# Optimization experiments

Hardware: AMD Instinct MI355X
Metric: run time of the kernel (lower is better)

Reference implementation:

```python
import jax, jax.numpy as jnp
import numpy as np

EPS_BN = 1e-5
EPS_LN = 1e-5

def _bn(x, gamma, beta, ch_axis):
    # training-mode BatchNorm: batch stats over all axes except ch_axis (biased var)
    axes = tuple(i for i in range(x.ndim) if i != ch_axis)
    mean = x.mean(axes, keepdims=True)
    var = x.var(axes, keepdims=True)
    shp = [1] * x.ndim; shp[ch_axis] = -1
    return (x - mean) / jnp.sqrt(var + EPS_BN) * gamma.reshape(shp) + beta.reshape(shp)

def _ln(x, gamma, beta):
    mean = x.mean(-1, keepdims=True)
    var = x.var(-1, keepdims=True)
    return (x - mean) / jnp.sqrt(var + EPS_LN) * gamma + beta

def _spline(x, knots, cps):
    # x: (B,S); knots, cps: (K,). Single-pass bucketize + gather + lerp,
    # equivalent to the torch per-interval masked loop (boundary points take
    # the right interval's t=0 value, identical result).
    K = knots.shape[0]
    xn = (x - jnp.min(x)) / (jnp.max(x) - jnp.min(x) + 1e-6)
    idx = jnp.clip(jnp.searchsorted(knots, xn, side='right') - 1, 0, K - 2)
    k0, k1 = knots[idx], knots[idx + 1]
    t = (xn - k0) / (k1 - k0)
    val = (1.0 - t) * cps[idx] + t * cps[idx + 1]
    in_range = (xn >= knots[0]) & (xn <= knots[-1])
    return jnp.where(in_range, val, 0.0)

def _mha(x, in_w, in_b, out_w, out_b, H):
    # torch nn.MultiheadAttention with batch_first=False: dim0 is the sequence.
    L, N, D = x.shape
    hd = D // H
    qkv = x @ in_w.T + in_b                       # (L,N,3D)
    q, k, v = jnp.split(qkv, 3, axis=-1)
    q = q.reshape(L, N, H, hd) * (1.0 / np.sqrt(hd))
    k = k.reshape(L, N, H, hd)
    v = v.reshape(L, N, H, hd)
    scores = jnp.einsum('lnhd,mnhd->nhlm', q, k)  # (N,H,L,L)
    attn = jax.nn.softmax(scores, axis=-1)
    out = jnp.einsum('nhlm,mnhd->lnhd', attn, v).reshape(L, N, D)
    return out @ out_w.T + out_b

def setup_inputs() -> dict:
    B, S, D, F, K, H = 32, 1024, 512, 8, 32, 8
    key = jax.random.key(0)
    ks = jax.random.split(key, 12)
    s = 0.02
    inp = {
        'x': jax.random.normal(ks[0], (B, S, D), jnp.float32),
        'in_w': jax.random.normal(ks[1], (3 * D, D), jnp.float32) * s,
        'in_b': jnp.zeros((3 * D,), jnp.float32),
        'out_w': jax.random.normal(ks[2], (D, D), jnp.float32) * s,
        'out_b': jnp.zeros((D,), jnp.float32),
        'attn_g': jnp.ones((D,), jnp.float32),
        'attn_beta': jnp.zeros((D,), jnp.float32),
        'proj_w': jax.random.normal(ks[3], (F, D), jnp.float32) * s,
        'proj_b': jnp.zeros((F,), jnp.float32),
        'pn_g': jnp.ones((F,), jnp.float32),
        'pn_beta': jnp.zeros((F,), jnp.float32),
        'knots': jnp.tile(jnp.linspace(0.0, 1.0, K, dtype=jnp.float32)[None, :], (F, 1)),
        'cps': jax.random.normal(ks[4], (F, K), jnp.float32) / np.sqrt(K),
        'gate_w': jax.random.normal(ks[5], (2 * D, F), jnp.float32) * s,
        'gate_b': jnp.zeros((2 * D,), jnp.float32),
        'gbn_g': jnp.ones((S,), jnp.float32),   # BatchNorm1d(2*d_model) hits dim1 = seq (= 2*d_model)
        'gbn_beta': jnp.zeros((S,), jnp.float32),
        'ln_g': jnp.ones((D,), jnp.float32),
        'ln_beta': jnp.zeros((D,), jnp.float32),
        'outp_w': jax.random.normal(ks[6], (D, D), jnp.float32) * s,
        'outp_b': jnp.zeros((D,), jnp.float32),
        'on_g': jnp.ones((D,), jnp.float32),
        'on_beta': jnp.zeros((D,), jnp.float32),
    }
    return inp

def reference(x, in_w, in_b, out_w, out_b, attn_g, attn_beta, proj_w, proj_b,
              pn_g, pn_beta, knots, cps, gate_w, gate_b, gbn_g, gbn_beta,
              ln_g, ln_beta, outp_w, outp_b, on_g, on_beta):
    H = 8
    attn_out = _mha(x, in_w, in_b, out_w, out_b, H)          # (B,S,D)
    attn_out = _bn(attn_out, attn_g, attn_beta, 2)
    projected = x @ proj_w.T + proj_b                         # (B,S,F)
    projected = _bn(projected, pn_g, pn_beta, 2)
    transformed = jax.vmap(_spline, in_axes=(2, 0, 0), out_axes=2)(projected, knots, cps)  # (B,S,F)
    h = transformed @ gate_w.T + gate_b                       # (B,S,2D)
    h = _bn(h, gbn_g, gbn_beta, 1)                            # channel axis = seq (torch quirk)
    a, b = jnp.split(h, 2, axis=-1)
    glu = a * jax.nn.sigmoid(b)                               # (B,S,D)
    gated = _ln(glu, ln_g, ln_beta)
    out = gated @ outp_w.T + outp_b
    out = _bn(out, on_g, on_beta, 2)
    return x + attn_out + out
```

## Files before the change

### kernel.cpp

```cpp
#include <hip/hip_runtime.h>
#include <math.h>


#define SOFF_AMEAN 0
#define SOFF_ARSTD 512
#define SOFF_OMEAN 1024
#define SOFF_ORSTD 1536
#define SOFF_PMEAN 2048
#define SOFF_PRSTD 2056
#define SOFF_FMIN  2064
#define SOFF_FMAX  2072
#define SOFF_SMEAN 2080
#define SOFF_SRSTD 3104
#define SOFF_G1    4128
#define SOFF_GB    4136
#define SOFF_SGB   4144
#define SOFF_QGB   4145
#define SOFF_G2    4160
#define SOFF_PART  4224

typedef short bf16x8_t __attribute__((ext_vector_type(8)));
typedef float f32x4_t __attribute__((ext_vector_type(4)));
typedef unsigned short us8_t __attribute__((ext_vector_type(8)));

__device__ __forceinline__ unsigned short f2bf(float f) {
  unsigned u = __float_as_uint(f);
  u = (u + 0x7FFFu + ((u >> 16) & 1u)) >> 16;
  return (unsigned short)u;
}
__device__ __forceinline__ float b2f(unsigned short u) {
  return __uint_as_float(((unsigned)u) << 16);
}

#define BARR do { asm volatile("" ::: "memory"); __builtin_amdgcn_s_barrier(); asm volatile("" ::: "memory"); } while (0)

__global__ __launch_bounds__(256) void zero_kernel(float* __restrict__ p) {
  p[blockIdx.x * 256 + threadIdx.x] = 0.f;
}

__global__ __launch_bounds__(256) void cvt8_kernel(const float* __restrict__ src,
                                                   unsigned short* __restrict__ dst) {
  int i = blockIdx.x * 256 + threadIdx.x;
  float4 a = ((const float4*)src)[i * 2];
  float4 b = ((const float4*)src)[i * 2 + 1];
  us8_t o;
  o[0] = f2bf(a.x); o[1] = f2bf(a.y); o[2] = f2bf(a.z); o[3] = f2bf(a.w);
  o[4] = f2bf(b.x); o[5] = f2bf(b.y); o[6] = f2bf(b.z); o[7] = f2bf(b.w);
  *(us8_t*)(dst + (size_t)i * 8) = o;
}

template<int NT, bool OUT_BF16, bool STATS>
__global__ __launch_bounds__(512, 2) void gemm256_kernel(
    const unsigned short* __restrict__ A, const unsigned short* __restrict__ B,
    const float* __restrict__ bias, unsigned short* __restrict__ Cb,
    float* __restrict__ Cf, float* __restrict__ gstats, int N) {
  __shared__ unsigned short As[4][256 * 32];
  __shared__ unsigned short Bs[4][256 * 32];
  const int bi = blockIdx.x;
  const int xcd = bi & 7, jb = bi >> 3;
  const int m0 = (xcd * 16 + jb / NT) * 256;
  const int n0 = (jb % NT) * 256;
  const int t = threadIdx.x;
  const int w = t >> 6, lane = t & 63;
  const int wm = w >> 2, wn = w & 3;

  const unsigned short* gA = A + (size_t)(m0 + w * 16 + (lane >> 2)) * 512
                               + (((lane & 3) ^ ((lane >> 3) & 3)) * 8);
  const unsigned short* gB = B + (size_t)(n0 + w * 16 + (lane >> 2)) * 512
                               + (((lane & 3) ^ ((lane >> 3) & 3)) * 8);

  const int fr = lane & 15, g = lane >> 4;
  const int kf = (fr >> 1) & 3;

  f32x4_t acc[8][4];
#pragma unroll
  for (int i = 0; i < 8; ++i)
#pragma unroll
    for (int jj = 0; jj < 4; ++jj) acc[i][jj] = (f32x4_t){0.f, 0.f, 0.f, 0.f};

#define STAGE(KT) do { \
    __builtin_amdgcn_global_load_lds( \
        (const __attribute__((address_space(1))) void*)(gA + (KT) * 32), \
        (__attribute__((address_space(3))) void*)&As[(KT) & 3][(w * 16) * 32], 16, 0, 0); \
    __builtin_amdgcn_global_load_lds( \
        (const __attribute__((address_space(1))) void*)(gA + (KT) * 32 + 128 * 512), \
        (__attribute__((address_space(3))) void*)&As[(KT) & 3][(128 + w * 16) * 32], 16, 0, 0); \
    __builtin_amdgcn_global_load_lds( \
        (const __attribute__((address_space(1))) void*)(gB + (KT) * 32), \
        (__attribute__((address_space(3))) void*)&Bs[(KT) & 3][(w * 16) * 32], 16, 0, 0); \
    __builtin_amdgcn_global_load_lds( \
        (const __attribute__((address_space(1))) void*)(gB + (KT) * 32 + 128 * 512), \
        (__attribute__((address_space(3))) void*)&Bs[(KT) & 3][(128 + w * 16) * 32], 16, 0, 0); \
  } while (0)

  STAGE(0); STAGE(1); STAGE(2);
  asm volatile("s_waitcnt vmcnt(8)" ::: "memory");
  BARR;

#pragma unroll
  for (int kt = 0; kt < 16; ++kt) {
    if (kt < 13) STAGE(kt + 3);
    const unsigned short* asb = &As[kt & 3][0];
    const unsigned short* bsb = &Bs[kt & 3][0];
    bf16x8_t af[8], bf[4];
#pragma unroll
    for (int ni = 0; ni < 4; ++ni)
      bf[ni] = *(const bf16x8_t*)&bsb[(wn * 64 + ni * 16 + fr) * 32 + ((g ^ kf) * 8)];
#pragma unroll
    for (int mi = 0; mi < 8; ++mi)
      af[mi] = *(const bf16x8_t*)&asb[(wm * 128 + mi * 16 + fr) * 32 + ((g ^ kf) * 8)];
    __builtin_amdgcn_s_setprio(1);
#pragma unroll
    for (int mi = 0; mi < 8; ++mi)
#pragma unroll
      for (int ni = 0; ni < 4; ++ni)
        acc[mi][ni] = __builtin_amdgcn_mfma_f32_16x16x32_bf16(af[mi], bf[ni], acc[mi][ni], 0, 0, 0);
    __builtin_amdgcn_s_setprio(0);
    if (kt < 15) {
      if (kt <= 12)      asm volatile("s_waitcnt vmcnt(8)" ::: "memory");
      else if (kt == 13) asm volatile("s_waitcnt vmcnt(4)" ::: "memory");
      else               asm volatile("s_waitcnt vmcnt(0)" ::: "memory");
      BARR;
    }
  }
#undef STAGE

  const int cr = (lane >> 4) * 4, cc = lane & 15;
  float bv[4], lsum[4], lsq[4];
#pragma unroll
  for (int ni = 0; ni < 4; ++ni) {
    bv[ni] = bias[n0 + wn * 64 + ni * 16 + cc];
    lsum[ni] = 0.f; lsq[ni] = 0.f;
  }
#pragma unroll
  for (int mi = 0; mi < 8; ++mi) {
#pragma unroll
    for (int jj = 0; jj < 4; ++jj) {
      const size_t row = (size_t)(m0 + wm * 128 + mi * 16 + cr + jj);
#pragma unroll
      for (int ni = 0; ni < 4; ++ni) {
        int col = n0 + wn * 64 + ni * 16 + cc;
        float v = acc[mi][ni][jj] + bv[ni];
        if (OUT_BF16) Cb[row * N + col] = f2bf(v);
        else          Cf[row * N + col] = v;
        if (STATS) { lsum[ni] += v; lsq[ni] += v * v; }
      }
    }
  }
  if (STATS) {
#pragma unroll
    for (int ni = 0; ni < 4; ++ni) {
      float s = lsum[ni], q = lsq[ni];
      s += __shfl_xor(s, 16); s += __shfl_xor(s, 32);
      q += __shfl_xor(q, 16); q += __shfl_xor(q, 32);
      if (lane < 16) {
        int col = n0 + wn * 64 + ni * 16 + lane;
        atomicAdd(&gstats[col], s);
        atomicAdd(&gstats[512 + col], q);
      }
    }
  }
}

__global__ __launch_bounds__(512) void statsfin_kernel(const float* __restrict__ part,
                                                       float* __restrict__ stats, int off) {
  int t = threadIdx.x;
  float mean = part[t] / 32768.f;
  float var = part[512 + t] / 32768.f - mean * mean;
  stats[off + t] = mean;
  stats[off + 512 + t] = rsqrtf(var + 1e-5f);
}

__global__ __launch_bounds__(256) void attn2_kernel(const unsigned short* __restrict__ qkv,
                                                    unsigned short* __restrict__ ctxb) {
  const int n = blockIdx.x, h = blockIdx.y, t = threadIdx.x;
  __shared__ float qs[32 * 68], ks[32 * 68], vs[32 * 68], ss[32 * 33];
  const int l = t >> 3, j0 = (t & 7) * 8;
  size_t rowb = ((size_t)(l * 1024 + n)) * 1536 + h * 64 + j0;
  us8_t qv = *(const us8_t*)(qkv + rowb);
  us8_t kv = *(const us8_t*)(qkv + rowb + 512);
  us8_t vv = *(const us8_t*)(qkv + rowb + 1024);
#pragma unroll
  for (int j = 0; j < 8; ++j) {
    qs[l * 68 + j0 + j] = b2f(qv[j]) * 0.125f;
    ks[l * 68 + j0 + j] = b2f(kv[j]);
    vs[l * 68 + j0 + j] = b2f(vv[j]);
  }
  __syncthreads();
  for (int o = t; o < 1024; o += 256) {
    int ll = o >> 5, m = o & 31;
    const float4* q4 = (const float4*)&qs[ll * 68];
    const float4* k4 = (const float4*)&ks[m * 68];
    float s = 0.f;
#pragma unroll
    for (int dd = 0; dd < 16; ++dd) {
      float4 a = q4[dd], b = k4[dd];
      s += a.x * b.x + a.y * b.y + a.z * b.z + a.w * b.w;
    }
    ss[ll * 33 + m] = s;
  }
  __syncthreads();
  if (t < 32) {
    float mx = -3e38f;
    for (int m = 0; m < 32; ++m) mx = fmaxf(mx, ss[t * 33 + m]);
    float sum = 0.f;
    for (int m = 0; m < 32; ++m) { float e = __expf(ss[t * 33 + m] - mx); ss[t * 33 + m] = e; sum += e; }
    float inv = 1.f / sum;
    for (int m = 0; m < 32; ++m) ss[t * 33 + m] *= inv;
  }
  __syncthreads();
  float o[8] = {0.f, 0.f, 0.f, 0.f, 0.f, 0.f, 0.f, 0.f};
#pragma unroll 8
  for (int m = 0; m < 32; ++m) {
    float pm = ss[l * 33 + m];
    const float* vr = &vs[m * 68 + j0];
#pragma unroll
    for (int j = 0; j < 8; ++j) o[j] += pm * vr[j];
  }
  us8_t ov;
#pragma unroll
  for (int j = 0; j < 8; ++j) ov[j] = f2bf(o[j]);
  *(us8_t*)(ctxb + ((size_t)(l * 1024 + n)) * 512 + h * 64 + j0) = ov;
}

__global__ __launch_bounds__(256) void proj_kernel(const float* __restrict__ x,
    const float* __restrict__ pw, const float* __restrict__ pb, float* __restrict__ p) {
  int blk = blockIdx.x, t = threadIdx.x;
  int r0 = blk * 64;
  __shared__ float xsp[64 * 33];
  __shared__ float pwc[8 * 33];
  int l = t >> 2, fg = t & 3;
  float acc0 = 0.f, acc1 = 0.f;
  for (int k0 = 0; k0 < 512; k0 += 32) {
    __syncthreads();
    for (int i = t; i < 2048; i += 256) { int ll = i >> 5, kk = i & 31; xsp[ll * 33 + kk] = x[(size_t)(r0 + ll) * 512 + k0 + kk]; }
    { int ff = t >> 5, kk = t & 31; pwc[ff * 33 + kk] = pw[ff * 512 + k0 + kk]; }
    __syncthreads();
#pragma unroll 8
    for (int kk = 0; kk < 32; ++kk) {
      float xv = xsp[l * 33 + kk];
      acc0 += xv * pwc[(fg * 2) * 33 + kk];
      acc1 += xv * pwc[(fg * 2 + 1) * 33 + kk];
    }
  }
  float2 o; o.x = acc0 + pb[fg * 2]; o.y = acc1 + pb[fg * 2 + 1];
  *(float2*)&p[(r0 + l) * 8 + fg * 2] = o;
}

__global__ __launch_bounds__(256) void projstats_kernel(const float* __restrict__ p,
                                                        float* __restrict__ part) {
  int t = threadIdx.x, blk = blockIdx.x;
  int f = t & 7;
  float s = 0.f, s2 = 0.f;
  for (int r = blk * 32 + (t >> 3); r < 32768; r += 2048) { float v = p[r * 8 + f]; s += v; s2 += v * v; }
  __shared__ float red[256], red2[256];
  red[t] = s; red2[t] = s2; __syncthreads();
  for (int off = 128; off >= 8; off >>= 1) { if (t < off) { red[t] += red[t + off]; red2[t] += red2[t + off]; } __syncthreads(); }
  if (t < 8) { part[blk * 16 + t] = red[t]; part[blk * 16 + 8 + t] = red2[t]; }
}
__global__ void projfin_kernel(const float* __restrict__ part, float* __restrict__ stats) {
  int t = threadIdx.x;
  if (t < 8) {
    float s = 0.f, s2 = 0.f;
    for (int b = 0; b < 64; ++b) { s += part[b * 16 + t]; s2 += part[b * 16 + 8 + t]; }
    float mean = s / 32768.f;
    float var = s2 / 32768.f - mean * mean;
    stats[SOFF_PMEAN + t] = mean;
    stats[SOFF_PRSTD + t] = rsqrtf(var + 1e-5f);
  }
}

__global__ __launch_bounds__(256) void bnminmax_kernel(float* __restrict__ p,
    const float* __restrict__ stats, const float* __restrict__ png,
    const float* __restrict__ pnb, float* __restrict__ part) {
  int t = threadIdx.x, blk = blockIdx.x;
  int i0 = blk * 256 + t;
  int f = i0 & 7;
  float k1 = stats[SOFF_PRSTD + f] * png[f];
  float k0 = pnb[f] - stats[SOFF_PMEAN + f] * k1;
  float mn = 3e38f, mx = -3e38f;
  for (int i = i0; i < 262144; i += 16384) {
    float v = p[i] * k1 + k0;
    p[i] = v;
    mn = fminf(mn, v); mx = fmaxf(mx, v);
  }
  __shared__ float rmn[256], rmx[256];
  rmn[t] = mn; rmx[t] = mx; __syncthreads();
  for (int off = 128; off >= 8; off >>= 1) {
    if (t < off) { rmn[t] = fminf(rmn[t], rmn[t + off]); rmx[t] = fmaxf(rmx[t], rmx[t + off]); }
    __syncthreads();
  }
  if (t < 8) { part[blk * 16 + t] = rmn[t]; part[blk * 16 + 8 + t] = rmx[t]; }
}
__global__ void minmaxfin_kernel(const float* __restrict__ part, float* __restrict__ stats) {
  int t = threadIdx.x;
  if (t < 8) {
    float mn = 3e38f, mx = -3e38f;
    for (int b = 0; b < 64; ++b) { mn = fminf(mn, part[b * 16 + t]); mx = fmaxf(mx, part[b * 16 + 8 + t]); }
    stats[SOFF_FMIN + t] = mn;
    stats[SOFF_FMAX + t] = mx;
  }
}

__global__ __launch_bounds__(256) void spline_kernel(float* __restrict__ p,
    const float* __restrict__ knots, const float* __restrict__ cps,
    const float* __restrict__ stats) {
  __shared__ float ksh[8 * 33], csh[8 * 33];
  int t = threadIdx.x;
  { int f = t >> 5, j = t & 31; ksh[f * 33 + j] = knots[t]; csh[f * 33 + j] = cps[t]; }
  __syncthreads();
  int i = blockIdx.x * 256 + t;
  int f = i & 7;
  float xv = p[i];
  float mn = stats[SOFF_FMIN + f], mx = stats[SOFF_FMAX + f];
  float xn = (xv - mn) / (mx - mn + 1e-6f);
  const float* kn = &ksh[f * 33];
  const float* cp = &csh[f * 33];
  int pcnt = 0;
#pragma unroll
  for (int j = 0; j < 32; ++j) pcnt += (kn[j] <= xn) ? 1 : 0;
  int idx = pcnt - 1;
  idx = idx < 0 ? 0 : (idx > 30 ? 30 : idx);
  float k0v = kn[idx], k1v = kn[idx + 1];
  float tt = (xn - k0v) / (k1v - k0v);
  float val = (1.f - tt) * cp[idx] + tt * cp[idx + 1];
  bool inr = (xn >= kn[0]) && (xn <= kn[31]);
  p[i] = inr ? val : 0.f;
}

__global__ __launch_bounds__(256) void gateprep_kernel(const float* __restrict__ gw,
    const float* __restrict__ gb, float* __restrict__ stats) {
  int b = blockIdx.x, t = threadIdx.x;
  __shared__ float red[256];
  float s = 0.f;
  if (b < 64) {
    int f1 = b >> 3, f2 = b & 7;
    for (int j = t; j < 1024; j += 256) s += gw[j * 8 + f1] * gw[j * 8 + f2];
  } else if (b < 72) {
    int f = b - 64;
    for (int j = t; j < 1024; j += 256) s += gw[j * 8 + f];
  } else if (b < 80) {
    int f = b - 72;
    for (int j = t; j < 1024; j += 256) s += gb[j] * gw[j * 8 + f];
  } else if (b == 80) {
    for (int j = t; j < 1024; j += 256) s += gb[j];
  } else {
    for (int j = t; j < 1024; j += 256) s += gb[j] * gb[j];
  }
  red[t] = s; __syncthreads();
  for (int off = 128; off > 0; off >>= 1) { if (t < off) red[t] += red[t + off]; __syncthreads(); }
  if (t == 0) {
    float v = red[0];
    if (b < 64) stats[SOFF_G2 + b] = v;
    else if (b < 72) stats[SOFF_G1 + (b - 64)] = v;
    else if (b < 80) stats[SOFF_GB + (b - 72)] = v;
    else if (b == 80) stats[SOFF_SGB] = v;
    else stats[SOFF_QGB] = v;
  }
}

__global__ __launch_bounds__(256) void sstats_kernel(const float* __restrict__ tbuf,
                                                     float* __restrict__ stats) {
  int s = blockIdx.x, t = threadIdx.x;
  __shared__ float tv[256];
  __shared__ float red[256];
  __shared__ float T1[8];
  __shared__ float Ms[64];
  int b = t >> 3, f = t & 7;
  tv[t] = tbuf[(b * 1024 + s) * 8 + f];
  __syncthreads();
  red[t] = tv[t]; __syncthreads();
  for (int off = 128; off >= 8; off >>= 1) { if (t < off) red[t] += red[t + off]; __syncthreads(); }
  if (t < 8) T1[t] = red[t];
  if (t < 64) {
    int f1 = t >> 3, f2 = t & 7; float sM = 0.f;
    for (int bb = 0; bb < 32; ++bb) sM += tv[bb * 8 + f1] * tv[bb * 8 + f2];
    Ms[t] = sM;
  }
  __syncthreads();
  if (t == 0) {
    float sh = 0.f, s2 = 0.f;
    for (int ff = 0; ff < 8; ++ff) {
      sh += stats[SOFF_G1 + ff] * T1[ff];
      s2 += 2.f * stats[SOFF_GB + ff] * T1[ff];
    }
    sh += 32.f * stats[SOFF_SGB];
    for (int i = 0; i < 64; ++i) s2 += Ms[i] * stats[SOFF_G2 + i];
    s2 += 32.f * stats[SOFF_QGB];
    float mean = sh / 32768.f;
    float var = s2 / 32768.f - mean * mean;
    stats[SOFF_SMEAN + s] = mean;
    stats[SOFF_SRSTD + s] = rsqrtf(var + 1e-5f);
  }
}

__global__ __launch_bounds__(256) void gluln_kernel(const float* __restrict__ tbuf,
    const float* __restrict__ gw, const float* __restrict__ gb,
    const float* __restrict__ stats, const float* __restrict__ gbng,
    const float* __restrict__ gbnb, const float* __restrict__ lng,
    const float* __restrict__ lnb, unsigned short* __restrict__ gatedb) {
  const int t = threadIdx.x, wave = t >> 6, lane = t & 63;
  for (int rr = 0; rr < 4; ++rr) {
    const int r = blockIdx.x * 16 + wave * 4 + rr;
    const int s = r & 1023;
    float4 tA = *(const float4*)&tbuf[r * 8];
    float4 tB = *(const float4*)&tbuf[r * 8 + 4];
    float smean = stats[SOFF_SMEAN + s], srstd = stats[SOFF_SRSTD + s];
    float k1 = srstd * gbng[s];
    float k0 = gbnb[s] - smean * k1;
    float g[8];
    float sum = 0.f, sq = 0.f;
#pragma unroll
    for (int i = 0; i < 8; ++i) {
      int c = i * 64 + lane;
      float4 wa0 = *(const float4*)&gw[c * 8];
      float4 wa1 = *(const float4*)&gw[c * 8 + 4];
      float4 wb0 = *(const float4*)&gw[(c + 512) * 8];
      float4 wb1 = *(const float4*)&gw[(c + 512) * 8 + 4];
      float ha = tA.x * wa0.x + tA.y * wa0.y + tA.z * wa0.z + tA.w * wa0.w
               + tB.x * wa1.x + tB.y * wa1.y + tB.z * wa1.z + tB.w * wa1.w + gb[c];
      float hb = tA.x * wb0.x + tA.y * wb0.y + tA.z * wb0.z + tA.w * wb0.w
               + tB.x * wb1.x + tB.y * wb1.y + tB.z * wb1.z + tB.w * wb1.w + gb[c + 512];
      ha = ha * k1 + k0;
      hb = hb * k1 + k0;
      float gv = ha / (1.f + __expf(-hb));
      g[i] = gv; sum += gv; sq += gv * gv;
    }
#pragma unroll
    for (int m = 32; m >= 1; m >>= 1) { sum += __shfl_xor(sum, m); sq += __shfl_xor(sq, m); }
    float mean = sum * (1.f / 512.f);
    float rstd = rsqrtf(sq * (1.f / 512.f) - mean * mean + 1e-5f);
#pragma unroll
    for (int i = 0; i < 8; ++i) {
      int c = i * 64 + lane;
      gatedb[(size_t)r * 512 + c] = f2bf((g[i] - mean) * rstd * lng[c] + lnb[c]);
    }
  }
}

__global__ __launch_bounds__(256) void final_kernel(const float* __restrict__ x,
    const float* __restrict__ attn, const float* __restrict__ outl,
    const float* __restrict__ stats, const float* __restrict__ ag,
    const float* __restrict__ ab, const float* __restrict__ og,
    const float* __restrict__ ob, float* __restrict__ y) {
  int idx = blockIdx.x * 256 + threadIdx.x;
  int c4 = (idx & 127) * 4;
  float4 xv = ((const float4*)x)[idx];
  float4 av = ((const float4*)attn)[idx];
  float4 ov = ((const float4*)outl)[idx];
  float4 am = *(const float4*)&stats[SOFF_AMEAN + c4];
  float4 ar = *(const float4*)&stats[SOFF_ARSTD + c4];
  float4 om = *(const float4*)&stats[SOFF_OMEAN + c4];
  float4 orr = *(const float4*)&stats[SOFF_ORSTD + c4];
  float4 g1 = *(const float4*)&ag[c4];
  float4 b1 = *(const float4*)&ab[c4];
  float4 g2 = *(const float4*)&og[c4];
  float4 b2 = *(const float4*)&ob[c4];
  float4 o;
  o.x = xv.x + (av.x - am.x) * ar.x * g1.x + b1.x + (ov.x - om.x) * orr.x * g2.x + b2.x;
  o.y = xv.y + (av.y - am.y) * ar.y * g1.y + b1.y + (ov.y - om.y) * orr.y * g2.y + b2.y;
  o.z = xv.z + (av.z - am.z) * ar.z * g1.z + b1.z + (ov.z - om.z) * orr.z * g2.z + b2.z;
  o.w = xv.w + (av.w - am.w) * ar.w * g1.w + b1.w + (ov.w - om.w) * orr.w * g2.w + b2.w;
  ((float4*)y)[idx] = o;
}

extern "C" void kernel_launch(void* const* d_in, const int* in_sizes, int n_in,
                              void* d_out, int out_size, void* d_ws, size_t ws_size,
                              hipStream_t stream) {
  (void)in_sizes; (void)n_in; (void)out_size; (void)ws_size;
  const float* x        = (const float*)d_in[0];
  const float* in_w     = (const float*)d_in[1];
  const float* in_b     = (const float*)d_in[2];
  const float* out_w    = (const float*)d_in[3];
  const float* out_b    = (const float*)d_in[4];
  const float* attn_g   = (const float*)d_in[5];
  const float* attn_bt  = (const float*)d_in[6];
  const float* proj_w   = (const float*)d_in[7];
  const float* proj_b   = (const float*)d_in[8];
  const float* pn_g     = (const float*)d_in[9];
  const float* pn_bt    = (const float*)d_in[10];
  const float* knots    = (const float*)d_in[11];
  const float* cps      = (const float*)d_in[12];
  const float* gate_w   = (const float*)d_in[13];
  const float* gate_b   = (const float*)d_in[14];
  const float* gbn_g    = (const float*)d_in[15];
  const float* gbn_bt   = (const float*)d_in[16];
  const float* ln_g     = (const float*)d_in[17];
  const float* ln_bt    = (const float*)d_in[18];
  const float* outp_w   = (const float*)d_in[19];
  const float* outp_b   = (const float*)d_in[20];
  const float* on_g     = (const float*)d_in[21];
  const float* on_bt    = (const float*)d_in[22];

  float* out = (float*)d_out;
  unsigned short* xb      = (unsigned short*)d_ws;
  unsigned short* qkv_b   = xb + 16777216;
  unsigned short* ctx_b   = qkv_b + 50331648;
  unsigned short* wqkv_b  = ctx_b + 16777216;
  unsigned short* wout_b  = wqkv_b + 786432;
  unsigned short* woutp_b = wout_b + 262144;
  float* proj  = (float*)(woutp_b + 262144);
  float* stats = proj + 262144;
  float* part  = stats + SOFF_PART;
  float* partA  = part;
  float* partO  = part + 1024;
  float* partP  = part + 2048;
  float* partMM = part + 3072;
  float* attnf = (float*)qkv_b;
  unsigned short* gated_b = xb;

  zero_kernel<<<dim3(8), dim3(256), 0, stream>>>(part);
  cvt8_kernel<<<dim3(8192), dim3(256), 0, stream>>>(x, xb);
  cvt8_kernel<<<dim3(384), dim3(256), 0, stream>>>(in_w, wqkv_b);
  cvt8_kernel<<<dim3(128), dim3(256), 0, stream>>>(out_w, wout_b);
  cvt8_kernel<<<dim3(128), dim3(256), 0, stream>>>(outp_w, woutp_b);
  gemm256_kernel<6, true, false><<<dim3(768), dim3(512), 0, stream>>>(
      xb, wqkv_b, in_b, qkv_b, nullptr, nullptr, 1536);
  attn2_kernel<<<dim3(1024, 8), dim3(256), 0, stream>>>(qkv_b, ctx_b);
  gemm256_kernel<2, false, true><<<dim3(256), dim3(512), 0, stream>>>(
      ctx_b, wout_b, out_b, nullptr, attnf, partA, 512);
  statsfin_kernel<<<dim3(1), dim3(512), 0, stream>>>(partA, stats, SOFF_AMEAN);
  proj_kernel<<<dim3(512), dim3(256), 0, stream>>>(x, proj_w, proj_b, proj);
  projstats_kernel<<<dim3(64), dim3(256), 0, stream>>>(proj, partP);
  projfin_kernel<<<dim3(1), dim3(64), 0, stream>>>(partP, stats);
  bnminmax_kernel<<<dim3(64), dim3(256), 0, stream>>>(proj, stats, pn_g, pn_bt, partMM);
  minmaxfin_kernel<<<dim3(1), dim3(64), 0, stream>>>(partMM, stats);
  spline_kernel<<<dim3(1024), dim3(256), 0, stream>>>(proj, knots, cps, stats);
  gateprep_kernel<<<dim3(88), dim3(256), 0, stream>>>(gate_w, gate_b, stats);
  sstats_kernel<<<dim3(1024), dim3(256), 0, stream>>>(proj, stats);
  gluln_kernel<<<dim3(2048), dim3(256), 0, stream>>>(proj, gate_w, gate_b, stats,
                                                     gbn_g, gbn_bt, ln_g, ln_bt, gated_b);
  gemm256_kernel<2, false, true><<<dim3(256), dim3(512), 0, stream>>>(
      gated_b, woutp_b, outp_b, nullptr, out, partO, 512);
  statsfin_kernel<<<dim3(1), dim3(512), 0, stream>>>(partO, stats, SOFF_OMEAN);
  final_kernel<<<dim3(16384), dim3(256), 0, stream>>>(x, attnf, out, stats,
                                                      attn_g, attn_bt, on_g, on_bt, out);
}
```

Before: 522.5 us.

## Rewrite attention kernel as single-wavefront MFMA bf16 QK^T and PV

Replaces the 256-thread FP32 LDS-based attention kernel with a 64-lane single-wavefront kernel. It computes the 32x32 scores and the probability-times-V product with bf16 16x16x32 MFMA instructions, keeps Q and K fragments in registers, and transposes only V through a small LDS buffer. Softmax runs in registers using cross-lane shuffles, and the probabilities are repacked into MFMA operand layout with xor shuffles. This removes most LDS traffic and scalar FMA work per (batch, head) block. In exchange the probabilities are rounded to bf16, the lane-permutation logic is intricate, and the output stores are scattered 2-byte writes.

```diff
diff --git a/kernel.cpp b/kernel.cpp
--- a/kernel.cpp
+++ b/kernel.cpp
@@ -171,56 +171,120 @@
   stats[off + 512 + t] = rsqrtf(var + 1e-5f);
 }
 
-__global__ __launch_bounds__(256) void attn2_kernel(const unsigned short* __restrict__ qkv,
-                                                    unsigned short* __restrict__ ctxb) {
-  const int n = blockIdx.x, h = blockIdx.y, t = threadIdx.x;
-  __shared__ float qs[32 * 68], ks[32 * 68], vs[32 * 68], ss[32 * 33];
-  const int l = t >> 3, j0 = (t & 7) * 8;
-  size_t rowb = ((size_t)(l * 1024 + n)) * 1536 + h * 64 + j0;
-  us8_t qv = *(const us8_t*)(qkv + rowb);
-  us8_t kv = *(const us8_t*)(qkv + rowb + 512);
-  us8_t vv = *(const us8_t*)(qkv + rowb + 1024);
-#pragma unroll
-  for (int j = 0; j < 8; ++j) {
-    qs[l * 68 + j0 + j] = b2f(qv[j]) * 0.125f;
-    ks[l * 68 + j0 + j] = b2f(kv[j]);
-    vs[l * 68 + j0 + j] = b2f(vv[j]);
-  }
+__global__ __launch_bounds__(64) void attn3_kernel(const unsigned short* __restrict__ qkv,
+                                                   unsigned short* __restrict__ ctxb) {
+  const int n = blockIdx.x, h = blockIdx.y;
+  const int lane = threadIdx.x;
+  const int fr = lane & 15, g = lane >> 4;
+  const int r = lane & 31, hi2 = lane >> 5;
+  __shared__ unsigned short vt[64 * 32];
+
+  const unsigned short* base = qkv + (size_t)n * 1536 + (size_t)h * 64;
+
+#pragma unroll
+  for (int i = 0; i < 4; ++i) {
+    const int d0 = (i * 2 + hi2) * 8;
+    union { us8_t v; unsigned u[4]; } ov;
+    ov.v = *(const us8_t*)(base + (size_t)r * 1572864 + 1024 + d0);
+#pragma unroll
+    for (int w = 0; w < 4; ++w) {
+      unsigned o = ov.u[w];
+      unsigned pu = __shfl_xor(o, 1);
+      unsigned val = (r & 1) ? ((pu >> 16) | (o & 0xFFFF0000u))
+                             : ((o & 0xFFFFu) | (pu << 16));
+      int dw = d0 + 2 * w + (r & 1);
+      *(unsigned*)&vt[dw * 32 + (r >> 1) * 2] = val;
+    }
+  }
+
+  bf16x8_t kfr[2][2], qfr[2][2];
+#pragma unroll
+  for (int mi = 0; mi < 2; ++mi)
+#pragma unroll
+    for (int s = 0; s < 2; ++s)
+      kfr[mi][s] = *(const bf16x8_t*)(base + (size_t)(mi * 16 + fr) * 1572864 + 512 + s * 32 + g * 8);
+#pragma unroll
+  for (int li = 0; li < 2; ++li)
+#pragma unroll
+    for (int s = 0; s < 2; ++s)
+      qfr[li][s] = *(const bf16x8_t*)(base + (size_t)(li * 16 + fr) * 1572864 + s * 32 + g * 8);
+
+  f32x4_t st[2][2];
+#pragma unroll
+  for (int mi = 0; mi < 2; ++mi)
+#pragma unroll
+    for (int li = 0; li < 2; ++li) {
+      st[mi][li] = (f32x4_t){0.f, 0.f, 0.f, 0.f};
+#pragma unroll
+      for (int s = 0; s < 2; ++s)
+        st[mi][li] = __builtin_amdgcn_mfma_f32_16x16x32_bf16(kfr[mi][s], qfr[li][s], st[mi][li], 0, 0, 0);
+    }
+
   __syncthreads();
-  for (int o = t; o < 1024; o += 256) {
-    int ll = o >> 5, m = o & 31;
-    const float4* q4 = (const float4*)&qs[ll * 68];
-    const float4* k4 = (const float4*)&ks[m * 68];
-    float s = 0.f;
-#pragma unroll
-    for (int dd = 0; dd < 16; ++dd) {
-      float4 a = q4[dd], b = k4[dd];
-      s += a.x * b.x + a.y * b.y + a.z * b.z + a.w * b.w;
-    }
-    ss[ll * 33 + m] = s;
-  }
-  __syncthreads();
-  if (t < 32) {
+  bf16x8_t vf[4];
+#pragma unroll
+  for (int dj = 0; dj < 4; ++dj)
+    vf[dj] = *(const bf16x8_t*)&vt[(dj * 16 + fr) * 32 + g * 8];
+
+  const bool pj = (g & 1) != 0, hb = (g >> 1) != 0;
+  f32x4_t outacc[2][4];
+#pragma unroll
+  for (int li = 0; li < 2; ++li) {
     float mx = -3e38f;
-    for (int m = 0; m < 32; ++m) mx = fmaxf(mx, ss[t * 33 + m]);
-    float sum = 0.f;
-    for (int m = 0; m < 32; ++m) { float e = __expf(ss[t * 33 + m] - mx); ss[t * 33 + m] = e; sum += e; }
-    float inv = 1.f / sum;
-    for (int m = 0; m < 32; ++m) ss[t * 33 + m] *= inv;
-  }
-  __syncthreads();
-  float o[8] = {0.f, 0.f, 0.f, 0.f, 0.f, 0.f, 0.f, 0.f};
-#pragma unroll 8
-  for (int m = 0; m < 32; ++m) {
-    float pm = ss[l * 33 + m];
-    const float* vr = &vs[m * 68 + j0];
-#pragma unroll
-    for (int j = 0; j < 8; ++j) o[j] += pm * vr[j];
-  }
-  us8_t ov;
-#pragma unroll
-  for (int j = 0; j < 8; ++j) ov[j] = f2bf(o[j]);
-  *(us8_t*)(ctxb + ((size_t)(l * 1024 + n)) * 512 + h * 64 + j0) = ov;
+#pragma unroll
+    for (int mi = 0; mi < 2; ++mi)
+#pragma unroll
+      for (int rr = 0; rr < 4; ++rr) mx = fmaxf(mx, st[mi][li][rr]);
+    mx = fmaxf(mx, __shfl_xor(mx, 16));
+    mx = fmaxf(mx, __shfl_xor(mx, 32));
+    float e[2][4]; float sm = 0.f;
+#pragma unroll
+    for (int mi = 0; mi < 2; ++mi)
+#pragma unroll
+      for (int rr = 0; rr < 4; ++rr) {
+        float ev = __expf((st[mi][li][rr] - mx) * 0.125f);
+        e[mi][rr] = ev; sm += ev;
+      }
+    sm += __shfl_xor(sm, 16);
+    sm += __shfl_xor(sm, 32);
+    float inv = 1.f / sm;
+    unsigned ww00 = ((unsigned)f2bf(e[0][1] * inv) << 16) | f2bf(e[0][0] * inv);
+    unsigned ww01 = ((unsigned)f2bf(e[0][3] * inv) << 16) | f2bf(e[0][2] * inv);
+    unsigned ww10 = ((unsigned)f2bf(e[1][1] * inv) << 16) | f2bf(e[1][0] * inv);
+    unsigned ww11 = ((unsigned)f2bf(e[1][3] * inv) << 16) | f2bf(e[1][2] * inv);
+    unsigned pw00 = __shfl_xor(ww00, 16), pw01 = __shfl_xor(ww01, 16);
+    unsigned pw10 = __shfl_xor(ww10, 16), pw11 = __shfl_xor(ww11, 16);
+    unsigned s00 = pj ? (hb ? pw00 : pw10) : (hb ? ww00 : ww10);
+    unsigned s01 = pj ? (hb ? pw01 : pw11) : (hb ? ww01 : ww11);
+    unsigned s10 = pj ? (hb ? ww00 : ww10) : (hb ? pw00 : pw10);
+    unsigned s11 = pj ? (hb ? ww01 : ww11) : (hb ? pw01 : pw11);
+    unsigned sb00 = __shfl_xor(s00, 32), sb01 = __shfl_xor(s01, 32);
+    unsigned sb10 = __shfl_xor(s10, 32), sb11 = __shfl_xor(s11, 32);
+    unsigned k00 = pj ? (hb ? pw10 : pw00) : (hb ? ww10 : ww00);
+    unsigned k01 = pj ? (hb ? pw11 : pw01) : (hb ? ww11 : ww01);
+    unsigned k10 = pj ? (hb ? ww10 : ww00) : (hb ? pw10 : pw00);
+    unsigned k11 = pj ? (hb ? ww11 : ww01) : (hb ? pw11 : pw01);
+    const bool take = (pj != hb);
+    union { unsigned u[4]; bf16x8_t v; } pa;
+    pa.u[0] = take ? sb00 : k00;
+    pa.u[1] = take ? sb01 : k01;
+    pa.u[2] = take ? sb10 : k10;
+    pa.u[3] = take ? sb11 : k11;
+#pragma unroll
+    for (int dj = 0; dj < 4; ++dj)
+      outacc[li][dj] = __builtin_amdgcn_mfma_f32_16x16x32_bf16(
+          pa.v, vf[dj], (f32x4_t){0.f, 0.f, 0.f, 0.f}, 0, 0, 0);
+  }
+
+#pragma unroll
+  for (int li = 0; li < 2; ++li)
+#pragma unroll
+    for (int dj = 0; dj < 4; ++dj)
+#pragma unroll
+      for (int rr = 0; rr < 4; ++rr) {
+        int l = li * 16 + g * 4 + rr;
+        ctxb[((size_t)l * 1024 + n) * 512 + h * 64 + dj * 16 + fr] = f2bf(outacc[li][dj][rr]);
+      }
 }
 
 __global__ __launch_bounds__(256) void proj_kernel(const float* __restrict__ x,
@@ -516,7 +580,7 @@
   cvt8_kernel<<<dim3(128), dim3(256), 0, stream>>>(outp_w, woutp_b);
   gemm256_kernel<6, true, false><<<dim3(768), dim3(512), 0, stream>>>(
       xb, wqkv_b, in_b, qkv_b, nullptr, nullptr, 1536);
-  attn2_kernel<<<dim3(1024, 8), dim3(256), 0, stream>>>(qkv_b, ctx_b);
+  attn3_kernel<<<dim3(1024, 8), dim3(64), 0, stream>>>(qkv_b, ctx_b);
   gemm256_kernel<2, false, true><<<dim3(256), dim3(512), 0, stream>>>(
       ctx_b, wout_b, out_b, nullptr, attnf, partA, 512);
   statsfin_kernel<<<dim3(1), dim3(512), 0, stream>>>(partA, stats, SOFF_AMEAN);
```

Result: faster. 470.3 us (-10.0%).
